# Optimization experiments

Measured on AMD Instinct MI355X. Metric: run time of the kernel, lower is better.

The kernel has to match this reference:

```python
import jax, jax.numpy as jnp
import numpy as np

WS = (2, 7, 7)    # window_size (t,h,w)
SS = (1, 3, 3)    # shift_size
HEADS = 4


def _rel_pos_index(ws):
    t, h, w = ws
    coords = np.stack(np.meshgrid(np.arange(t), np.arange(h), np.arange(w), indexing='ij'))
    cf = coords.reshape(3, -1)                       # (3, N)
    rc = (cf[:, :, None] - cf[:, None, :]).transpose(1, 2, 0).astype(np.int64)  # (N,N,3)
    rc[:, :, 0] += t - 1
    rc[:, :, 1] += h - 1
    rc[:, :, 2] += w - 1
    rc[:, :, 0] *= (2 * h - 1) * (2 * w - 1)
    rc[:, :, 1] *= (2 * w - 1)
    return rc.sum(-1)                                # (N,N) int


def _compute_mask(Tp, Hp, Wp, ws, ss, dtype):
    img = np.zeros((1, Tp, Hp, Wp, 1), np.float32)
    cnt = 0
    for d in (slice(-ws[0]), slice(-ws[0], -ss[0]), slice(-ss[0], None)):
        for hh in (slice(-ws[1]), slice(-ws[1], -ss[1]), slice(-ss[1], None)):
            for ww in (slice(-ws[2]), slice(-ws[2], -ss[2]), slice(-ss[2], None)):
                img[:, d, hh, ww, :] = cnt
                cnt += 1
    t, h, w = ws
    m = img.reshape(1, Tp // t, t, Hp // h, h, Wp // w, w, 1)
    m = m.transpose(0, 1, 3, 5, 2, 4, 6, 7).reshape(-1, t * h * w)  # (nW, N)
    am = m[:, None, :] - m[:, :, None]
    return jnp.asarray(np.where(am != 0, -100.0, 0.0), dtype)        # (nW, N, N)


def setup_inputs() -> dict:
    key = jax.random.key(0)
    k0, k1, k2, k3 = jax.random.split(key, 4)
    B, T, H, W, C = 2, 16, 56, 56, 128
    x = jax.random.normal(k0, (B, T, H, W, C), jnp.float32)
    qkv_w = jax.random.normal(k1, (3 * C, C), jnp.float32) * (C ** -0.5)
    proj_w = jax.random.normal(k2, (C, C), jnp.float32) * (C ** -0.5)
    proj_b = jnp.zeros((C,), jnp.float32)
    tbl = (2 * WS[0] - 1) * (2 * WS[1] - 1) * (2 * WS[2] - 1)  # 507
    rpb_table = jax.random.normal(k3, (tbl, HEADS), jnp.float32) * 0.02
    return {"x": x, "qkv_w": qkv_w, "proj_w": proj_w, "proj_b": proj_b, "rpb_table": rpb_table}


def _forward(x, qkv_w, proj_w, proj_b, rpb_table):
    B, T, H, W, C = x.shape
    ws, ss = list(WS), list(SS)
    for i, d in enumerate((T, H, W)):
        if d <= ws[i]:
            ws[i] = d
            ss[i] = 0
    t, h, w = ws
    dims = (T, H, W)
    pad = [(ws[i] - dims[i] % ws[i]) % ws[i] for i in range(3)]
    x = jnp.pad(x, ((0, 0), (0, pad[0]), (0, pad[1]), (0, pad[2]), (0, 0)))
    Tp, Hp, Wp = x.shape[1], x.shape[2], x.shape[3]
    shifted = any(s > 0 for s in ss)
    if shifted:
        x = jnp.roll(x, (-ss[0], -ss[1], -ss[2]), (1, 2, 3))
        mask = _compute_mask(Tp, Hp, Wp, ws, ss, x.dtype)  # (nW, N, N)
    else:
        mask = None
    # window partition -> (B_, N, C)
    xw = x.reshape(B, Tp // t, t, Hp // h, h, Wp // w, w, C)
    xw = xw.transpose(0, 1, 3, 5, 2, 4, 6, 7).reshape(-1, t * h * w, C)
    B_, N, _ = xw.shape
    hd = C // HEADS
    scale = hd ** -0.5
    qkv = (xw @ qkv_w.T).reshape(B_, N, 3, HEADS, hd).transpose(2, 0, 3, 1, 4)
    q, k, v = qkv[0] * scale, qkv[1], qkv[2]           # (B_, heads, N, hd)
    attn = jnp.einsum('bhnd,bhmd->bhnm', q, k)
    rpi = _rel_pos_index(tuple(ws))[:N, :N].reshape(-1)
    bias = rpb_table[rpi].reshape(N, N, HEADS).transpose(2, 0, 1)  # (heads, N, N)
    attn = attn + bias[None]
    if mask is not None:
        nW = mask.shape[0]
        attn = attn.reshape(B_ // nW, nW, HEADS, N, N) + mask[None, :, None]
        attn = attn.reshape(-1, HEADS, N, N)
    attn = jax.nn.softmax(attn, axis=-1)
    out = jnp.einsum('bhnm,bhmd->bnhd', attn, v).reshape(B_, N, C)
    out = out @ proj_w.T + proj_b
    # window reverse (faithful to original, including swapped h/w in the view)
    xr = out.reshape(B, Tp // t, Hp // h, Wp // w, t, w, h, C)
    xr = xr.transpose(0, 1, 4, 2, 5, 3, 6, 7).reshape(B, Tp, Hp, Wp, C)
    if shifted:
        xr = jnp.roll(xr, (ss[0], ss[1], ss[2]), (1, 2, 3))
    return xr[:, :T, :H, :W, :]


def reference(x, qkv_w, proj_w, proj_b, rpb_table):
    return _forward(x, qkv_w, proj_w, proj_b, rpb_table)
```

## Files before the change

kernel.cpp:

```cpp
#include <hip/hip_runtime.h>
#include <hip/hip_bf16.h>

typedef __bf16 bf16x8 __attribute__((ext_vector_type(8)));
typedef __bf16 bf16x4 __attribute__((ext_vector_type(4)));
typedef float  f32x4  __attribute__((ext_vector_type(4)));

#define MFMA16(A,B,C) __builtin_amdgcn_mfma_f32_16x16x32_bf16((A),(B),(C),0,0,0)

constexpr int LK  = 0;
constexpr int LV  = 35840;
constexpr int LP  = 0;
constexpr int LO  = 16384;
constexpr int LQS = 45056;
constexpr int LDS_BYTES = 73728;

__device__ __forceinline__ bf16x8 cvt8(float4 a, float4 b) {
    bf16x8 r;
    r[0]=(__bf16)a.x; r[1]=(__bf16)a.y; r[2]=(__bf16)a.z; r[3]=(__bf16)a.w;
    r[4]=(__bf16)b.x; r[5]=(__bf16)b.y; r[6]=(__bf16)b.z; r[7]=(__bf16)b.w;
    return r;
}

__global__ void swin_addt_kernel(const float* __restrict__ rpb, float* __restrict__ addT) {
    int idx = blockIdx.x * 256 + threadIdx.x;
    if (idx >= 8*4*112*112) return;
    int i   = idx % 112;
    int j   = (idx / 112) % 112;
    int h   = (idx / (112*112)) & 3;
    int cls = idx / (112*112*4);
    float v;
    if (j >= 98) v = -1e30f;
    else if (i >= 98) v = 0.0f;
    else {
        int ti = i / 49, ri = i % 49, hi = ri / 7, wi = ri % 7;
        int tj = j / 49, rj = j % 49, hj = rj / 7, wj = rj % 7;
        int rel = (ti - tj + 1)*169 + (hi - hj + 6)*13 + (wi - wj + 6);
        v = rpb[rel*4 + h];
        int rt_i = (cls & 4) ? (1 + ti) : 0;
        int rh_i = (cls & 2) ? ((hi < 4) ? 1 : 2) : 0;
        int rw_i = (cls & 1) ? ((wi < 4) ? 1 : 2) : 0;
        int rt_j = (cls & 4) ? (1 + tj) : 0;
        int rh_j = (cls & 2) ? ((hj < 4) ? 1 : 2) : 0;
        int rw_j = (cls & 1) ? ((wj < 4) ? 1 : 2) : 0;
        if (rt_i*9 + rh_i*3 + rw_i != rt_j*9 + rh_j*3 + rw_j) v -= 100.0f;
    }
    addT[idx] = v;
}

__global__ __launch_bounds__(256, 2)
void swin_fused_kernel(const float* __restrict__ x, const float* __restrict__ qkv_w,
                       const float* __restrict__ proj_w, const float* __restrict__ proj_b,
                       const float* __restrict__ addT, float* __restrict__ out) {
    __shared__ __align__(16) unsigned char smem[LDS_BYTES];
    const int tid  = threadIdx.x;
    const int lane = tid & 63;
    const int wv   = tid >> 6;
    const int l15  = lane & 15;
    const int l4   = lane >> 4;

    const int win  = blockIdx.x;
    const int b    = win >> 9;
    const int wr   = win & 511;
    const int bt   = wr >> 6, bh = (wr >> 3) & 7, bw = wr & 7;
    const int cls  = ((bt==7)?4:0) | ((bh==7)?2:0) | ((bw==7)?1:0);

    const f32x4 fz = {0.f, 0.f, 0.f, 0.f};

    for (int i = tid; i < 4*32*16; i += 256) {
        int n  = 112 + (i & 15);
        int d  = (i >> 4) & 31;
        int hh = i >> 9;
        *(__bf16*)(smem + LV + ((hh*32 + d) << 8) + ((2*n) ^ ((d & 7) << 4))) = (__bf16)0.0f;
    }

    bf16x8 wfr[6][4];
    for (int cs = 0; cs < 6; ++cs) {
        int part = cs >> 1;
        int row  = part*128 + wv*32 + ((cs & 1) << 4) + l15;
        const float* wp = qkv_w + row*128 + l4*8;
        for (int ks = 0; ks < 4; ++ks)
            wfr[cs][ks] = cvt8(*(const float4*)(wp + ks*32), *(const float4*)(wp + ks*32 + 4));
    }
    const float kscale = 0.17677669529663687f;
    bf16x8 q_save[7];
    #pragma unroll
    for (int mt = 0; mt < 7; ++mt) {
        int n  = mt*16 + l15;
        int it = n / 49; int rr = n - it*49; int ih = rr / 7; int iw = rr - ih*7;
        int ts = (bt*2 + it + 1) & 15;
        int hs = bh*7 + ih + 3; if (hs >= 56) hs -= 56;
        int vs = bw*7 + iw + 3; if (vs >= 56) vs -= 56;
        const float* xp = x + (((b*16 + ts)*56 + hs)*56 + vs)*128 + l4*8;
        bf16x8 afr[4];
        for (int ks = 0; ks < 4; ++ks)
            afr[ks] = cvt8(*(const float4*)(xp + ks*32), *(const float4*)(xp + ks*32 + 4));
        f32x4 acc[6];
        for (int cs = 0; cs < 6; ++cs) acc[cs] = fz;
        for (int ks = 0; ks < 4; ++ks)
            for (int cs = 0; cs < 6; ++cs)
                acc[cs] = MFMA16(afr[ks], wfr[cs][ks], acc[cs]);
        bf16x8 qs;
        #pragma unroll
        for (int r = 0; r < 4; ++r) {
            qs[r]     = (__bf16)(acc[0][r] * kscale);
            qs[r + 4] = (__bf16)(acc[1][r] * kscale);
        }
        q_save[mt] = qs;
        #pragma unroll
        for (int cs = 2; cs < 6; ++cs) {
            int part = cs >> 1;
            int d    = ((cs & 1) << 4) + l15;
            for (int r = 0; r < 4; ++r) {
                int nn = mt*16 + l4*4 + r;
                float v = acc[cs][r];
                if (part == 1)
                    *(__bf16*)(smem + LK + (wv*112 + nn)*80 + d*2) = (__bf16)v;
                else
                    *(__bf16*)(smem + LV + ((wv*32 + d) << 8) + ((2*nn) ^ ((d & 7) << 4))) = (__bf16)v;
            }
        }
    }
    __syncthreads();

    bf16x8 kfr[7];
    for (int nt = 0; nt < 7; ++nt)
        kfr[nt] = *(const bf16x8*)(smem + LK + (wv*112 + nt*16 + l15)*80 + l4*16);
    bf16x8 vfr[4][2];
    for (int ks = 0; ks < 4; ++ks)
        for (int dt = 0; dt < 2; ++dt) {
            int d = dt*16 + l15;
            vfr[ks][dt] = *(const bf16x8*)(smem + LV + ((wv*32 + d) << 8) + ((2*(ks*32 + l4*8)) ^ ((d & 7) << 4)));
        }
    __syncthreads();

    #pragma unroll
    for (int t = 0; t < 7; ++t) {
        bf16x8 qs = q_save[t];
        #pragma unroll
        for (int e = 0; e < 8; ++e) {
            int token = l4*4 + (e & 3);
            int d     = ((e >> 2) << 4) + l15;
            *(__bf16*)(smem + LQS + wv*7168 + t*1024 + token*64 + d*2) = qs[e];
        }
    }
    {
        int row = l15, col = 112 + l4*4;
        bf16x4 z4; z4[0]=z4[1]=z4[2]=z4[3]=(__bf16)0.0f;
        *(bf16x4*)(smem + LP + wv*4096 + row*256 + ((2*col) ^ ((row & 7) << 4))) = z4;
    }
    const float* at = addT + (cls*4 + wv)*112*112;
    for (int mt = 0; mt < 7; ++mt) {
        bf16x8 qfr = *(const bf16x8*)(smem + LQS + wv*7168 + mt*1024 + l15*64 + l4*16);
        f32x4 s[7];
        for (int nt = 0; nt < 7; ++nt) s[nt] = MFMA16(qfr, kfr[nt], fz);
        for (int nt = 0; nt < 7; ++nt)
            s[nt] += *(const f32x4*)(at + (nt*16 + l15)*112 + mt*16 + l4*4);
        float mx[4], sum[4];
        for (int r = 0; r < 4; ++r) {
            float m = s[0][r];
            for (int nt = 1; nt < 7; ++nt) m = fmaxf(m, s[nt][r]);
            m = fmaxf(m, __shfl_xor(m, 1));
            m = fmaxf(m, __shfl_xor(m, 2));
            m = fmaxf(m, __shfl_xor(m, 4));
            m = fmaxf(m, __shfl_xor(m, 8));
            mx[r] = m; sum[r] = 0.f;
        }
        for (int nt = 0; nt < 7; ++nt)
            for (int r = 0; r < 4; ++r) {
                float p = __expf(s[nt][r] - mx[r]);
                s[nt][r] = p;
                sum[r]  += p;
            }
        for (int r = 0; r < 4; ++r) {
            sum[r] += __shfl_xor(sum[r], 1);
            sum[r] += __shfl_xor(sum[r], 2);
            sum[r] += __shfl_xor(sum[r], 4);
            sum[r] += __shfl_xor(sum[r], 8);
        }
        for (int nt = 0; nt < 7; ++nt)
            for (int r = 0; r < 4; ++r) {
                int prow = l4*4 + r, pcol = nt*16 + l15;
                *(__bf16*)(smem + LP + wv*4096 + prow*256 + ((2*pcol) ^ ((prow & 7) << 4))) = (__bf16)s[nt][r];
            }
        f32x4 o0 = fz, o1 = fz;
        for (int ks = 0; ks < 4; ++ks) {
            bf16x8 pfr = *(const bf16x8*)(smem + LP + wv*4096 + l15*256 + ((ks*64 + l4*16) ^ ((l15 & 7) << 4)));
            o0 = MFMA16(pfr, vfr[ks][0], o0);
            o1 = MFMA16(pfr, vfr[ks][1], o1);
        }
        for (int r = 0; r < 4; ++r) {
            int nn = mt*16 + l4*4 + r;
            float inv = 1.0f / sum[r];
            int c0 = wv*32 + l15;
            *(__bf16*)(smem + LO + nn*256 + ((2*c0) ^ ((nn & 7) << 4)))      = (__bf16)(o0[r] * inv);
            *(__bf16*)(smem + LO + nn*256 + ((2*(c0+16)) ^ ((nn & 7) << 4))) = (__bf16)(o1[r] * inv);
        }
    }
    __syncthreads();

    bf16x8 pw[2][4];
    float  pb[2];
    for (int nt2 = 0; nt2 < 2; ++nt2) {
        int c = wv*32 + nt2*16 + l15;
        const float* wp = proj_w + c*128 + l4*8;
        for (int ks = 0; ks < 4; ++ks)
            pw[nt2][ks] = cvt8(*(const float4*)(wp + ks*32), *(const float4*)(wp + ks*32 + 4));
        pb[nt2] = proj_b[c];
    }
    for (int mt = 0; mt < 7; ++mt) {
        bf16x8 afr[4];
        int arow = mt*16 + l15;
        for (int ks = 0; ks < 4; ++ks)
            afr[ks] = *(const bf16x8*)(smem + LO + arow*256 + ((ks*64 + l4*16) ^ ((arow & 7) << 4)));
        f32x4 a0 = fz, a1 = fz;
        for (int ks = 0; ks < 4; ++ks) {
            a0 = MFMA16(afr[ks], pw[0][ks], a0);
            a1 = MFMA16(afr[ks], pw[1][ks], a1);
        }
        for (int r = 0; r < 4; ++r) {
            int nn = mt*16 + l4*4 + r;
            if (nn >= 98) continue;
            int it = nn / 49; int rr = nn - it*49; int ih = rr / 7; int iw = rr - ih*7;
            int td = (bt*2 + it + 1) & 15;
            int hd = bh*7 + ih + 3; if (hd >= 56) hd -= 56;
            int wd = bw*7 + iw + 3; if (wd >= 56) wd -= 56;
            float* op = out + (((b*16 + td)*56 + hd)*56 + wd)*128;
            op[wv*32 + l15]      = a0[r] + pb[0];
            op[wv*32 + 16 + l15] = a1[r] + pb[1];
        }
    }
}

extern "C" void kernel_launch(void* const* d_in, const int* in_sizes, int n_in,
                              void* d_out, int out_size, void* d_ws, size_t ws_size,
                              hipStream_t stream) {
    const float* x      = (const float*)d_in[0];
    const float* qkv_w  = (const float*)d_in[1];
    const float* proj_w = (const float*)d_in[2];
    const float* proj_b = (const float*)d_in[3];
    const float* rpb    = (const float*)d_in[4];
    float* out  = (float*)d_out;
    float* addT = (float*)d_ws;

    swin_addt_kernel<<<(8*4*112*112 + 255)/256, 256, 0, stream>>>(rpb, addT);
    swin_fused_kernel<<<1024, 256, 0, stream>>>(x, qkv_w, proj_w, proj_b, addT, out);
}
```

Baseline: 181.4 us.

## Split token tiles across two wave groups per head with 512-thread blocks

Doubles the block to 8 waves, assigning each head to two waves that split the 7 query token tiles (4 and 3). Q staging in LDS is reduced to a per-tile 1KB buffer written just before use, and the LDS layout is repacked to shrink the footprint. This aims to raise wave-level parallelism and latency hiding per window, at the cost of duplicated weight-fragment loads per head and tighter register limits from the new launch bounds.

Result: slower. 475.9 us (+162.4%).

```diff
diff --git a/kernel.cpp b/kernel.cpp
--- a/kernel.cpp
+++ b/kernel.cpp
@@ -10,9 +10,9 @@
 constexpr int LK  = 0;
 constexpr int LV  = 35840;
 constexpr int LP  = 0;
-constexpr int LO  = 16384;
-constexpr int LQS = 45056;
-constexpr int LDS_BYTES = 73728;
+constexpr int LO  = 32768;
+constexpr int LQS = 61440;
+constexpr int LDS_BYTES = 69632;
 
 __device__ __forceinline__ bf16x8 cvt8(float4 a, float4 b) {
     bf16x8 r;
@@ -47,14 +47,17 @@
     addT[idx] = v;
 }
 
-__global__ __launch_bounds__(256, 2)
+__global__ __launch_bounds__(512, 4)
 void swin_fused_kernel(const float* __restrict__ x, const float* __restrict__ qkv_w,
                        const float* __restrict__ proj_w, const float* __restrict__ proj_b,
                        const float* __restrict__ addT, float* __restrict__ out) {
     __shared__ __align__(16) unsigned char smem[LDS_BYTES];
-    const int tid  = threadIdx.x;
-    const int lane = tid & 63;
-    const int wv   = tid >> 6;
+    const int tid   = threadIdx.x;
+    const int lane  = tid & 63;
+    const int wv    = tid >> 6;
+    const int head  = wv & 3;
+    const int mtbeg = (wv >> 2) * 4;
+    const int mtcnt = (wv >> 2) ? 3 : 4;
     const int l15  = lane & 15;
     const int l4   = lane >> 4;
 
@@ -66,7 +69,7 @@
 
     const f32x4 fz = {0.f, 0.f, 0.f, 0.f};
 
-    for (int i = tid; i < 4*32*16; i += 256) {
+    for (int i = tid; i < 4*32*16; i += 512) {
         int n  = 112 + (i & 15);
         int d  = (i >> 4) & 31;
         int hh = i >> 9;
@@ -76,15 +79,17 @@
     bf16x8 wfr[6][4];
     for (int cs = 0; cs < 6; ++cs) {
         int part = cs >> 1;
-        int row  = part*128 + wv*32 + ((cs & 1) << 4) + l15;
+        int row  = part*128 + head*32 + ((cs & 1) << 4) + l15;
         const float* wp = qkv_w + row*128 + l4*8;
         for (int ks = 0; ks < 4; ++ks)
             wfr[cs][ks] = cvt8(*(const float4*)(wp + ks*32), *(const float4*)(wp + ks*32 + 4));
     }
     const float kscale = 0.17677669529663687f;
-    bf16x8 q_save[7];
+    bf16x8 q_save[4];
     #pragma unroll
-    for (int mt = 0; mt < 7; ++mt) {
+    for (int k = 0; k < 4; ++k) {
+        if (k >= mtcnt) break;
+        int mt = mtbeg + k;
         int n  = mt*16 + l15;
         int it = n / 49; int rr = n - it*49; int ih = rr / 7; int iw = rr - ih*7;
         int ts = (bt*2 + it + 1) & 15;
@@ -105,7 +110,7 @@
             qs[r]     = (__bf16)(acc[0][r] * kscale);
             qs[r + 4] = (__bf16)(acc[1][r] * kscale);
         }
-        q_save[mt] = qs;
+        q_save[k] = qs;
         #pragma unroll
         for (int cs = 2; cs < 6; ++cs) {
             int part = cs >> 1;
@@ -114,9 +119,9 @@
                 int nn = mt*16 + l4*4 + r;
                 float v = acc[cs][r];
                 if (part == 1)
-                    *(__bf16*)(smem + LK + (wv*112 + nn)*80 + d*2) = (__bf16)v;
+                    *(__bf16*)(smem + LK + (head*112 + nn)*80 + d*2) = (__bf16)v;
                 else
-                    *(__bf16*)(smem + LV + ((wv*32 + d) << 8) + ((2*nn) ^ ((d & 7) << 4))) = (__bf16)v;
+                    *(__bf16*)(smem + LV + ((head*32 + d) << 8) + ((2*nn) ^ ((d & 7) << 4))) = (__bf16)v;
             }
         }
     }
@@ -124,33 +129,35 @@
 
     bf16x8 kfr[7];
     for (int nt = 0; nt < 7; ++nt)
-        kfr[nt] = *(const bf16x8*)(smem + LK + (wv*112 + nt*16 + l15)*80 + l4*16);
+        kfr[nt] = *(const bf16x8*)(smem + LK + (head*112 + nt*16 + l15)*80 + l4*16);
     bf16x8 vfr[4][2];
     for (int ks = 0; ks < 4; ++ks)
         for (int dt = 0; dt < 2; ++dt) {
             int d = dt*16 + l15;
-            vfr[ks][dt] = *(const bf16x8*)(smem + LV + ((wv*32 + d) << 8) + ((2*(ks*32 + l4*8)) ^ ((d & 7) << 4)));
+            vfr[ks][dt] = *(const bf16x8*)(smem + LV + ((head*32 + d) << 8) + ((2*(ks*32 + l4*8)) ^ ((d & 7) << 4)));
         }
     __syncthreads();
 
-    #pragma unroll
-    for (int t = 0; t < 7; ++t) {
-        bf16x8 qs = q_save[t];
-        #pragma unroll
-        for (int e = 0; e < 8; ++e) {
-            int token = l4*4 + (e & 3);
-            int d     = ((e >> 2) << 4) + l15;
-            *(__bf16*)(smem + LQS + wv*7168 + t*1024 + token*64 + d*2) = qs[e];
-        }
-    }
     {
         int row = l15, col = 112 + l4*4;
         bf16x4 z4; z4[0]=z4[1]=z4[2]=z4[3]=(__bf16)0.0f;
         *(bf16x4*)(smem + LP + wv*4096 + row*256 + ((2*col) ^ ((row & 7) << 4))) = z4;
     }
-    const float* at = addT + (cls*4 + wv)*112*112;
-    for (int mt = 0; mt < 7; ++mt) {
-        bf16x8 qfr = *(const bf16x8*)(smem + LQS + wv*7168 + mt*1024 + l15*64 + l4*16);
+    const float* at = addT + (cls*4 + head)*112*112;
+    #pragma unroll
+    for (int k = 0; k < 4; ++k) {
+        if (k >= mtcnt) break;
+        int mt = mtbeg + k;
+        {
+            bf16x8 qs = q_save[k];
+            #pragma unroll
+            for (int e = 0; e < 8; ++e) {
+                int token = l4*4 + (e & 3);
+                int d     = ((e >> 2) << 4) + l15;
+                *(__bf16*)(smem + LQS + wv*1024 + token*64 + d*2) = qs[e];
+            }
+        }
+        bf16x8 qfr = *(const bf16x8*)(smem + LQS + wv*1024 + l15*64 + l4*16);
         f32x4 s[7];
         for (int nt = 0; nt < 7; ++nt) s[nt] = MFMA16(qfr, kfr[nt], fz);
         for (int nt = 0; nt < 7; ++nt)
@@ -191,7 +198,7 @@
         for (int r = 0; r < 4; ++r) {
             int nn = mt*16 + l4*4 + r;
             float inv = 1.0f / sum[r];
-            int c0 = wv*32 + l15;
+            int c0 = head*32 + l15;
             *(__bf16*)(smem + LO + nn*256 + ((2*c0) ^ ((nn & 7) << 4)))      = (__bf16)(o0[r] * inv);
             *(__bf16*)(smem + LO + nn*256 + ((2*(c0+16)) ^ ((nn & 7) << 4))) = (__bf16)(o1[r] * inv);
         }
@@ -201,13 +208,16 @@
     bf16x8 pw[2][4];
     float  pb[2];
     for (int nt2 = 0; nt2 < 2; ++nt2) {
-        int c = wv*32 + nt2*16 + l15;
+        int c = head*32 + nt2*16 + l15;
         const float* wp = proj_w + c*128 + l4*8;
         for (int ks = 0; ks < 4; ++ks)
             pw[nt2][ks] = cvt8(*(const float4*)(wp + ks*32), *(const float4*)(wp + ks*32 + 4));
         pb[nt2] = proj_b[c];
     }
-    for (int mt = 0; mt < 7; ++mt) {
+    #pragma unroll
+    for (int k = 0; k < 4; ++k) {
+        if (k >= mtcnt) break;
+        int mt = mtbeg + k;
         bf16x8 afr[4];
         int arow = mt*16 + l15;
         for (int ks = 0; ks < 4; ++ks)
@@ -225,8 +235,8 @@
             int hd = bh*7 + ih + 3; if (hd >= 56) hd -= 56;
             int wd = bw*7 + iw + 3; if (wd >= 56) wd -= 56;
             float* op = out + (((b*16 + td)*56 + hd)*56 + wd)*128;
-            op[wv*32 + l15]      = a0[r] + pb[0];
-            op[wv*32 + 16 + l15] = a1[r] + pb[1];
+            op[head*32 + l15]      = a0[r] + pb[0];
+            op[head*32 + 16 + l15] = a1[r] + pb[1];
         }
     }
 }
@@ -243,5 +253,5 @@
     float* addT = (float*)d_ws;
 
     swin_addt_kernel<<<(8*4*112*112 + 255)/256, 256, 0, stream>>>(rpb, addT);
-    swin_fused_kernel<<<1024, 256, 0, stream>>>(x, qkv_w, proj_w, proj_b, addT, out);
-}
+    swin_fused_kernel<<<1024, 512, 0, stream>>>(x, qkv_w, proj_w, proj_b, addT, out);
+}
```
